# Kernel optimization log

Hardware: AMD Instinct MI355X
Metric: run time of the kernel (lower is better)

Reference implementation:

```python
import jax, jax.numpy as jnp
import numpy as np

B, S, D, H, L = 4, 4096, 64, 8, 4
VOCAB, NCLS = 256, 10
MLP = D * H          # mlp_dim = dim * heads = 512
BS = 256             # block size for banded attention
R = 256              # one-sided radius (sliding_window_size = 512)


def sinusoid_pos_emb(s, d):
    pos = np.arange(s)[:, None].astype(np.float32)
    i = np.arange(d // 2)[None, :].astype(np.float32)
    ang = pos / np.power(10000.0, 2.0 * i / d)
    pe = np.zeros((s, d), np.float32)
    pe[:, 0::2] = np.sin(ang)
    pe[:, 1::2] = np.cos(ang)
    return jnp.asarray(pe)


def layernorm(x, s, b):
    m = x.mean(-1, keepdims=True)
    v = ((x - m) ** 2).mean(-1, keepdims=True)
    return (x - m) * jax.lax.rsqrt(v + 1e-6) * s + b


def sliding_window_attn(x, wq, bq, wk, bk, wv, bv, wo, bo):
    Bx, Sx, Dx = x.shape
    Dh = Dx // H
    nb = Sx // BS

    def proj(w, b2):
        return (x @ w + b2).reshape(Bx, Sx, H, Dh).transpose(0, 2, 1, 3)

    q = proj(wq, bq) / jnp.sqrt(jnp.float32(Dh))
    k = proj(wk, bk)
    v = proj(wv, bv)

    def windows(t):  # [B,H,S,Dh] -> [B,H,nb,3*BS,Dh] (prev | self | next blocks)
        tp = jnp.pad(t, ((0, 0), (0, 0), (BS, BS), (0, 0))).reshape(Bx, H, nb + 2, BS, Dh)
        return jnp.concatenate([tp[:, :, :-2], tp[:, :, 1:-1], tp[:, :, 2:]], axis=3)

    kw, vw = windows(k), windows(v)
    qb = q.reshape(Bx, H, nb, BS, Dh)
    scores = jnp.einsum('bhnqd,bhnkd->bhnqk', qb, kw)      # [B,H,nb,BS,3*BS]

    qpos = jnp.arange(BS)[:, None]
    kpos = jnp.arange(3 * BS)[None, :] - BS
    band = jnp.abs(kpos - qpos) <= R                        # [BS,3*BS]
    kglob = jnp.arange(nb)[:, None, None] * BS + kpos[None]  # [nb,1,3*BS]
    valid = (kglob >= 0) & (kglob < Sx)
    mask = band[None] & valid                                # [nb,BS,3*BS]

    scores = jnp.where(mask[None, None], scores, jnp.float32(-1e30))
    probs = jax.nn.softmax(scores, axis=-1)
    out = jnp.einsum('bhnqk,bhnkd->bhnqd', probs, vw)
    out = out.reshape(Bx, H, Sx, Dh).transpose(0, 2, 1, 3).reshape(Bx, Sx, Dx)
    return out @ wo + bo


def setup_inputs() -> dict:
    key = jax.random.key(0)
    ks = jax.random.split(key, 12)
    g = lambda k, shp: jax.random.normal(k, shp, dtype=jnp.float32) * 0.02
    emb = g(ks[0], (VOCAB, D)).at[0].set(0.0)  # padding_idx=0 row is zeros
    return dict(
        x=jax.random.randint(ks[1], (B, S), 0, VOCAB).astype(jnp.int32),
        emb=emb,
        wq=g(ks[2], (L, D, D)), bq=jnp.zeros((L, D)),
        wk=g(ks[3], (L, D, D)), bk=jnp.zeros((L, D)),
        wv=g(ks[4], (L, D, D)), bv=jnp.zeros((L, D)),
        wo=g(ks[5], (L, D, D)), bo=jnp.zeros((L, D)),
        ln1_s=jnp.ones((L, D)), ln1_b=jnp.zeros((L, D)),
        ln2_s=jnp.ones((L, D)), ln2_b=jnp.zeros((L, D)),
        w1=g(ks[6], (L, D, MLP)), b1=jnp.zeros((L, MLP)),
        w2=g(ks[7], (L, MLP, D)), b2=jnp.zeros((L, D)),
        lnf_s=jnp.ones((D,)), lnf_b=jnp.zeros((D,)),
        wcls=g(ks[8], (D, NCLS)), bcls=jnp.zeros((NCLS,)),
    )


def reference(x, emb, wq, bq, wk, bk, wv, bv, wo, bo, ln1_s, ln1_b, ln2_s, ln2_b, w1, b1, w2, b2, lnf_s, lnf_b, wcls, bcls):
    h = emb[x] + sinusoid_pos_emb(S, D)[None]                 # embedding + fixed pos emb
    for l in range(L):
        a = sliding_window_attn(layernorm(h, ln1_s[l], ln1_b[l]),
                                wq[l], bq[l], wk[l], bk[l], wv[l], bv[l], wo[l], bo[l])
        h = h + a
        y = layernorm(h, ln2_s[l], ln2_b[l])
        y = jax.nn.gelu(y @ w1[l] + b1[l]) @ w2[l] + b2[l]
        h = h + y
    h = layernorm(h, lnf_s, lnf_b)
    pooled = h.mean(axis=1)                                   # classifier_pool='MEAN'
    return pooled @ wcls + bcls
```

## Files before the change

kernel.cpp:

```cpp
#include <hip/hip_runtime.h>
#include <hip/hip_bf16.h>

#define DEV __device__ __forceinline__

typedef __attribute__((ext_vector_type(8))) short bf16x8;
typedef __attribute__((ext_vector_type(4))) float f32x4;
typedef __attribute__((ext_vector_type(16))) float f32x16;

DEV short f2bf(float x){ __hip_bfloat16 h = __float2bfloat16(x); return *(short*)&h; }
DEV unsigned pack2bf(float a, float b){
  return (unsigned)(unsigned short)f2bf(a) | ((unsigned)(unsigned short)f2bf(b) << 16);
}
DEV float gelu_fast(float x){
  float z = 0.7978845608028654f*(x + 0.044715f*x*x*x);
  float e = __expf(-2.f*z);
  return x / (1.f + e);
}

#define SB 4096
#define NT 16384
#define DM 64

__global__ __launch_bounds__(256) void wconv(
    const float* __restrict__ wq, const float* __restrict__ wk,
    const float* __restrict__ wv, const float* __restrict__ wo,
    const float* __restrict__ w1, const float* __restrict__ w2,
    short* __restrict__ wqT, short* __restrict__ wkT,
    short* __restrict__ wvT, short* __restrict__ woT,
    short* __restrict__ w1T, short* __restrict__ w2T)
{
  int t = blockIdx.x, l = blockIdx.y;
  const float* src; short* dst; int K, N, kt, nt;
  if (t < 16) {
    int m = t >> 2, sub = t & 3; kt = sub >> 1; nt = sub & 1; K = 64; N = 64;
    const float* s4[4] = {wq, wk, wv, wo};
    short*       d4[4] = {wqT, wkT, wvT, woT};
    src = s4[m] + l*4096; dst = d4[m] + l*4096;
  } else if (t < 48) {
    kt = (t-16) >> 4; nt = (t-16) & 15; K = 64; N = 512;
    src = w1 + l*32768; dst = w1T + l*32768;
  } else {
    kt = (t-48) >> 1; nt = (t-48) & 1; K = 512; N = 64;
    src = w2 + l*32768; dst = w2T + l*32768;
  }
  __shared__ float lds[32][33];
  int tx = threadIdx.x & 31, ty = threadIdx.x >> 5;
  int k0 = kt*32, n0 = nt*32;
  #pragma unroll
  for (int j=0;j<4;++j) lds[ty+8*j][tx] = src[(size_t)(k0+ty+8*j)*N + n0 + tx];
  __syncthreads();
  #pragma unroll
  for (int j=0;j<4;++j) {
    int nn = ty+8*j;
    dst[(size_t)(n0+nn)*K + k0 + tx] = f2bf(lds[tx][nn]);
  }
}

DEV void make_frags_ln(const float* rowp, float mean, float inv,
    const float* __restrict__ s, const float* __restrict__ b, int kq,
    bf16x8& a0, bf16x8& a1){
  #pragma unroll
  for (int i=0;i<8;++i) a0[i] = f2bf((rowp[kq*8+i]-mean)*inv*s[kq*8+i]+b[kq*8+i]);
  #pragma unroll
  for (int i=0;i<8;++i) a1[i] = f2bf((rowp[32+kq*8+i]-mean)*inv*s[32+kq*8+i]+b[32+kq*8+i]);
}

template<bool EMBED, bool LAST>
__global__ __launch_bounds__(512,2) void layer_kernel(
    const int* __restrict__ x, const float* __restrict__ emb,
    const unsigned short* __restrict__ qin, const unsigned short* __restrict__ kin,
    const unsigned short* __restrict__ vin,
    const short* __restrict__ woT, const float* __restrict__ bo,
    const float* __restrict__ ln2s, const float* __restrict__ ln2b,
    const short* __restrict__ w1T, const float* __restrict__ b1,
    const short* __restrict__ w2T, const float* __restrict__ b2,
    const float* __restrict__ lns, const float* __restrict__ lnb,
    const short* __restrict__ wqT, const short* __restrict__ wkT, const short* __restrict__ wvT,
    const float* __restrict__ bq, const float* __restrict__ bk, const float* __restrict__ bv,
    unsigned short* __restrict__ qo, unsigned short* __restrict__ ko, unsigned short* __restrict__ vo,
    float* __restrict__ h, float* __restrict__ part)
{
  __shared__ uint4 regA4[4608];
  __shared__ uint4 regB4[4672];
  __shared__ float mu[64], iv[64];

  unsigned short* Ks  = (unsigned short*)regA4;
  unsigned short* abL = (unsigned short*)regA4;
  float (*hN)[68]   = (float(*)[68])((char*)regA4 + 9216);
  float (*facc)[68] = (float(*)[68])((char*)regA4 + 26624);
  unsigned short* Vs = (unsigned short*)regB4;
  short (*mid)[520]  = (short(*)[520])regB4;

  const int bid = blockIdx.x;
  const int row_g0 = bid * 64;
  const int tid = threadIdx.x;
  const int w = tid >> 6, lane = tid & 63;
  const int r = lane & 15, kq = lane >> 4;
  const int srow = tid >> 3, sd8 = tid & 7;

  if constexpr (EMBED) {
    int tg = row_g0 + srow;
    int s = tg & (SB-1);
    int tok = x[tg];
    #pragma unroll
    for (int i=0;i<8;++i) {
      int d = sd8*8 + i;
      float fe = (float)(d & ~1) * (1.0f/64.0f);
      float invk = __expf(-9.210340371976184f * fe);
      float ang = (float)s * invk;
      float pe = (d & 1) ? __cosf(ang) : __sinf(ang);
      float val = emb[tok*DM + d] + pe;
      hN[srow][d] = val;
      h[(size_t)tg*DM + d] = val;
    }
  } else {
    const int bbase = row_g0 & ~(SB-1);
    const int kwin0 = row_g0 - 256;

    for (int idx = tid; idx < 4608; idx += 512) {
      int e = idx >> 3, grp = idx & 7;
      int g = kwin0 + e;
      uint4 kv = make_uint4(0,0,0,0), vv = make_uint4(0,0,0,0);
      if ((unsigned)(g - bbase) < (unsigned)SB) {
        kv = *(const uint4*)(kin + (size_t)g*DM + grp*8);
        vv = *(const uint4*)(vin + (size_t)g*DM + grp*8);
      }
      *(uint4*)(Ks + e*64 + ((grp ^ (e & 7)) << 3)) = kv;
      const unsigned short* pv = (const unsigned short*)&vv;
      #pragma unroll
      for (int d = 0; d < 8; ++d) Vs[(grp*8 + d)*584 + e] = pv[d];
    }
    __syncthreads();

    const int qc = lane & 31;
    const int hf = lane >> 5;

    auto attn_job = [&](int qs, f32x16& oacc, float& lacc) {
      const int qglob = row_g0 + qs*32 + qc;
      bf16x8 qfrag = {};
      if (hf == 0) qfrag = *(const bf16x8*)(qin + (size_t)qglob*DM + w*8);
      for (int t = 0; t <= 16; ++t) {
        const int k0l = qs*32 + 32*t;
        const int k0g = kwin0 + k0l;
        if (k0g > bbase + SB-1 || k0g + 31 < bbase) continue;

        bf16x8 kfrag = {};
        if (hf == 0) {
          int e = k0l + qc;
          kfrag = *(const bf16x8*)(Ks + e*64 + ((w ^ (e & 7)) << 3));
        }
        f32x16 s = __builtin_amdgcn_mfma_f32_32x32x16_bf16(kfrag, qfrag, (f32x16){}, 0, 0, 0);

        float pp[16];
        bool needmask = (t == 0) | (t == 16) | (k0g < bbase) | (k0g + 31 > bbase + SB-1);
        if (needmask) {
          #pragma unroll
          for (int rr = 0; rr < 16; ++rr) {
            int klg = k0g + (rr&3) + 8*(rr>>2) + 4*hf;
            bool ok = ((unsigned)(klg - qglob + 256) <= 512u) &&
                      ((unsigned)(klg - bbase) < (unsigned)SB);
            pp[rr] = ok ? __expf(s[rr]) : 0.f;
          }
        } else {
          #pragma unroll
          for (int rr = 0; rr < 16; ++rr) pp[rr] = __expf(s[rr]);
        }
        #pragma unroll
        for (int rr = 0; rr < 16; ++rr) lacc += pp[rr];

        unsigned pk[8];
        #pragma unroll
        for (int j = 0; j < 8; ++j) pk[j] = pack2bf(pp[2*j], pp[2*j+1]);
        unsigned sw[8];
        #pragma unroll
        for (int j = 0; j < 8; ++j) sw[j] = __shfl_xor(pk[j], 32, 64);

        union { unsigned u[4]; bf16x8 v; } pbA;
        pbA.u[0] = hf ? sw[2] : pk[0];
        pbA.u[1] = hf ? sw[3] : pk[1];
        pbA.u[2] = hf ? pk[2] : sw[0];
        pbA.u[3] = hf ? pk[3] : sw[1];
        bf16x8 va1 = {};
        if (qc < 8) va1 = *(const bf16x8*)(Vs + (w*8 + qc)*584 + k0l + 8*hf);
        oacc = __builtin_amdgcn_mfma_f32_32x32x16_bf16(va1, pbA.v, oacc, 0, 0, 0);

        union { unsigned u[4]; bf16x8 v; } pbB;
        pbB.u[0] = hf ? sw[6] : pk[4];
        pbB.u[1] = hf ? sw[7] : pk[5];
        pbB.u[2] = hf ? pk[6] : sw[4];
        pbB.u[3] = hf ? pk[7] : sw[5];
        bf16x8 va2 = {};
        if (qc < 8) va2 = *(const bf16x8*)(Vs + (w*8 + qc)*584 + k0l + 16 + 8*hf);
        oacc = __builtin_amdgcn_mfma_f32_32x32x16_bf16(va2, pbB.v, oacc, 0, 0, 0);
      }
    };

    f32x16 oacc0 = {}; float la0 = 0.f;
    f32x16 oacc1 = {}; float la1 = 0.f;
    attn_job(0, oacc0, la0);
    attn_job(1, oacc1, la1);
    float rcp0 = 1.f / (la0 + __shfl_xor(la0, 32, 64));
    float rcp1 = 1.f / (la1 + __shfl_xor(la1, 32, 64));
    __syncthreads();

    {
      unsigned short ov[4];
      #pragma unroll
      for (int j = 0; j < 4; ++j) ov[j] = (unsigned short)f2bf(oacc0[j] * rcp0);
      *(uint2*)(abL + (qc)*72 + w*8 + 4*hf) = *(uint2*)ov;
      #pragma unroll
      for (int j = 0; j < 4; ++j) ov[j] = (unsigned short)f2bf(oacc1[j] * rcp1);
      *(uint2*)(abL + (32 + qc)*72 + w*8 + 4*hf) = *(uint2*)ov;
    }
    __syncthreads();

    {
      const int rh = w >> 2, ct = w & 3;
      const int col = ct*16 + r;
      const short* wp = woT + (size_t)col*64 + kq*8;
      bf16x8 wb0 = *(const bf16x8*)(wp);
      bf16x8 wb1 = *(const bf16x8*)(wp + 32);
      #pragma unroll
      for (int rf=0; rf<2; ++rf) {
        const short* abp = (const short*)(abL + (rh*32 + rf*16 + r)*72 + kq*8);
        bf16x8 a0 = *(const bf16x8*)abp;
        bf16x8 a1 = *(const bf16x8*)(abp + 32);
        f32x4 acc = (f32x4){0.f,0.f,0.f,0.f};
        acc = __builtin_amdgcn_mfma_f32_16x16x32_bf16(a0, wb0, acc, 0, 0, 0);
        acc = __builtin_amdgcn_mfma_f32_16x16x32_bf16(a1, wb1, acc, 0, 0, 0);
        #pragma unroll
        for (int j=0;j<4;++j) {
          int rl = rh*32 + rf*16 + kq*4 + j;
          hN[rl][col] = acc[j] + bo[col] + h[(size_t)(row_g0+rl)*DM + col];
        }
      }
    }
  }
  __syncthreads();

  {
    const float* p = &hN[srow][sd8*8];
    float v[8];
    float sum = 0.f;
    #pragma unroll
    for (int i=0;i<8;++i){ v[i] = p[i]; sum += v[i]; }
    sum += __shfl_xor(sum, 1, 64); sum += __shfl_xor(sum, 2, 64); sum += __shfl_xor(sum, 4, 64);
    float mean = sum * (1.f/64.f);
    float sq = 0.f;
    #pragma unroll
    for (int i=0;i<8;++i){ float d = v[i]-mean; sq += d*d; }
    sq += __shfl_xor(sq, 1, 64); sq += __shfl_xor(sq, 2, 64); sq += __shfl_xor(sq, 4, 64);
    if (sd8 == 0) { mu[srow] = mean; iv[srow] = rsqrtf(sq*(1.f/64.f) + 1e-6f); }
  }
  __syncthreads();

  if constexpr (!EMBED) {
    {
      bf16x8 a[4][2];
      #pragma unroll
      for (int rf=0; rf<4; ++rf)
        make_frags_ln(&hN[rf*16 + r][0], mu[rf*16 + r], iv[rf*16 + r], ln2s, ln2b, kq, a[rf][0], a[rf][1]);
      const int gc0 = w*64;
      bf16x8 wb[4][2];
      #pragma unroll
      for (int ct=0; ct<4; ++ct) {
        const short* wp = w1T + (size_t)(gc0 + ct*16 + r)*64 + kq*8;
        wb[ct][0] = *(const bf16x8*)(wp);
        wb[ct][1] = *(const bf16x8*)(wp + 32);
      }
      f32x4 acc1[4][4];
      #pragma unroll
      for (int ct=0;ct<4;++ct)
        #pragma unroll
        for (int rf=0;rf<4;++rf) acc1[ct][rf] = (f32x4){0.f,0.f,0.f,0.f};
      #pragma unroll
      for (int ct=0; ct<4; ++ct)
        #pragma unroll
        for (int rf=0; rf<4; ++rf) {
          acc1[ct][rf] = __builtin_amdgcn_mfma_f32_16x16x32_bf16(a[rf][0], wb[ct][0], acc1[ct][rf], 0, 0, 0);
          acc1[ct][rf] = __builtin_amdgcn_mfma_f32_16x16x32_bf16(a[rf][1], wb[ct][1], acc1[ct][rf], 0, 0, 0);
        }
      __syncthreads();
      #pragma unroll
      for (int ct=0; ct<4; ++ct) {
        int gcol = gc0 + ct*16 + r;
        float bb = b1[gcol];
        #pragma unroll
        for (int rf=0; rf<4; ++rf)
          #pragma unroll
          for (int j=0; j<4; ++j)
            mid[rf*16 + kq*4 + j][gcol] = f2bf(gelu_fast(acc1[ct][rf][j] + bb));
      }
    }
    __syncthreads();

    {
      const int kh = w >> 2, ct2 = w & 3;
      const int col2 = ct2*16 + r;
      bf16x8 wf[8];
      #pragma unroll
      for (int ks=0; ks<8; ++ks)
        wf[ks] = *(const bf16x8*)(w2T + (size_t)col2*512 + kh*256 + ks*32 + kq*8);
      f32x4 acc2[4];
      #pragma unroll
      for (int rf=0;rf<4;++rf) acc2[rf] = (f32x4){0.f,0.f,0.f,0.f};
      #pragma unroll
      for (int ks=0; ks<8; ++ks)
        #pragma unroll
        for (int rf=0; rf<4; ++rf) {
          bf16x8 af = *(const bf16x8*)(&mid[rf*16 + r][kh*256 + ks*32 + kq*8]);
          acc2[rf] = __builtin_amdgcn_mfma_f32_16x16x32_bf16(af, wf[ks], acc2[rf], 0, 0, 0);
        }
      if (kh == 0) {
        #pragma unroll
        for (int rf=0; rf<4; ++rf)
          #pragma unroll
          for (int j=0;j<4;++j)
            facc[rf*16 + kq*4 + j][col2] = acc2[rf][j];
      }
      __syncthreads();
      if (kh == 1) {
        float bb = b2[col2];
        #pragma unroll
        for (int rf=0; rf<4; ++rf)
          #pragma unroll
          for (int j=0;j<4;++j) {
            int rl = rf*16 + kq*4 + j;
            float val = acc2[rf][j] + facc[rl][col2] + bb + hN[rl][col2];
            hN[rl][col2] = val;
            h[(size_t)(row_g0+rl)*DM + col2] = val;
          }
      }
    }
    __syncthreads();

    {
      const float* p = &hN[srow][sd8*8];
      float v[8];
      float sum = 0.f;
      #pragma unroll
      for (int i=0;i<8;++i){ v[i] = p[i]; sum += v[i]; }
      sum += __shfl_xor(sum, 1, 64); sum += __shfl_xor(sum, 2, 64); sum += __shfl_xor(sum, 4, 64);
      float mean = sum * (1.f/64.f);
      float sq = 0.f;
      #pragma unroll
      for (int i=0;i<8;++i){ float d = v[i]-mean; sq += d*d; }
      sq += __shfl_xor(sq, 1, 64); sq += __shfl_xor(sq, 2, 64); sq += __shfl_xor(sq, 4, 64);
      if (sd8 == 0) { mu[srow] = mean; iv[srow] = rsqrtf(sq*(1.f/64.f) + 1e-6f); }
    }
    __syncthreads();
  }

  if constexpr (!LAST) {
    const float qscale = 0.35355339059327373f;
    bf16x8 a[4][2];
    #pragma unroll
    for (int rf=0; rf<4; ++rf)
      make_frags_ln(&hN[rf*16 + r][0], mu[rf*16 + r], iv[rf*16 + r], lns, lnb, kq, a[rf][0], a[rf][1]);
    #pragma unroll
    for (int rep=0; rep<2; ++rep) {
      int jj = w + rep*8;
      if (jj < 12) {
        int m = jj >> 2, ct = jj & 3;
        const short* WT = m==0 ? wqT : (m==1 ? wkT : wvT);
        int col = ct*16 + r;
        const short* wp = WT + (size_t)col*64 + kq*8;
        bf16x8 wb0 = *(const bf16x8*)(wp);
        bf16x8 wb1 = *(const bf16x8*)(wp + 32);
        float bias = (m==0 ? bq : (m==1 ? bk : bv))[col];
        float scale = (m==0) ? qscale : 1.f;
        unsigned short* OPT = m==0 ? qo : (m==1 ? ko : vo);
        #pragma unroll
        for (int rf=0; rf<4; ++rf) {
          f32x4 acc = (f32x4){0.f,0.f,0.f,0.f};
          acc = __builtin_amdgcn_mfma_f32_16x16x32_bf16(a[rf][0], wb0, acc, 0, 0, 0);
          acc = __builtin_amdgcn_mfma_f32_16x16x32_bf16(a[rf][1], wb1, acc, 0, 0, 0);
          #pragma unroll
          for (int j=0;j<4;++j) {
            size_t oi = (size_t)(row_g0 + rf*16 + kq*4 + j)*DM + col;
            OPT[oi] = (unsigned short)f2bf((acc[j] + bias)*scale);
          }
        }
      }
    }
  } else {
    float mean = mu[srow], inv = iv[srow];
    #pragma unroll
    for (int i=0;i<8;++i) {
      int d = sd8*8 + i;
      hN[srow][d] = (hN[srow][d]-mean)*inv*lns[d] + lnb[d];
    }
    __syncthreads();
    if (tid < 64) {
      float s = 0.f;
      #pragma unroll 4
      for (int rr=0; rr<64; ++rr) s += hN[rr][tid];
      part[bid*64 + tid] = s;
    }
  }
}

__global__ __launch_bounds__(256) void pool_finalize(const float* __restrict__ part,
    const float* __restrict__ wcls, const float* __restrict__ bcls, float* __restrict__ out)
{
  int tid = threadIdx.x;
  int b = tid >> 6, d = tid & 63;
  float sum = 0.f;
  #pragma unroll 8
  for (int i = 0; i < 64; ++i) sum += part[(b*64 + i)*64 + d];
  __shared__ float pooled[4][64];
  pooled[b][d] = sum * (1.f/4096.f);
  __syncthreads();
  if (tid < 40) {
    int bb = tid / 10, c = tid % 10;
    float acc = bcls[c];
    #pragma unroll
    for (int dd = 0; dd < 64; ++dd) acc = fmaf(pooled[bb][dd], wcls[dd*10 + c], acc);
    out[tid] = acc;
  }
}

extern "C" void kernel_launch(void* const* d_in, const int* in_sizes, int n_in,
                              void* d_out, int out_size, void* d_ws, size_t ws_size,
                              hipStream_t stream)
{
  const int*   x    = (const int*)d_in[0];
  const float* emb  = (const float*)d_in[1];
  const float* wq   = (const float*)d_in[2];
  const float* bq   = (const float*)d_in[3];
  const float* wk   = (const float*)d_in[4];
  const float* bk   = (const float*)d_in[5];
  const float* wv   = (const float*)d_in[6];
  const float* bv   = (const float*)d_in[7];
  const float* wo   = (const float*)d_in[8];
  const float* bo   = (const float*)d_in[9];
  const float* ln1s = (const float*)d_in[10];
  const float* ln1b = (const float*)d_in[11];
  const float* ln2s = (const float*)d_in[12];
  const float* ln2b = (const float*)d_in[13];
  const float* w1   = (const float*)d_in[14];
  const float* b1   = (const float*)d_in[15];
  const float* w2   = (const float*)d_in[16];
  const float* b2   = (const float*)d_in[17];
  const float* lnfs = (const float*)d_in[18];
  const float* lnfb = (const float*)d_in[19];
  const float* wcls = (const float*)d_in[20];
  const float* bcls = (const float*)d_in[21];
  float* out = (float*)d_out;

  char* wsb = (char*)d_ws;
  const size_t MB = 1u << 20;
  float* h  = (float*)(wsb);
  unsigned short* qA = (unsigned short*)(wsb + 4*MB);
  unsigned short* kA = (unsigned short*)(wsb + 6*MB);
  unsigned short* vA = (unsigned short*)(wsb + 8*MB);
  unsigned short* qB = (unsigned short*)(wsb + 10*MB);
  unsigned short* kB = (unsigned short*)(wsb + 12*MB);
  unsigned short* vB = (unsigned short*)(wsb + 14*MB);
  short* wqT = (short*)(wsb + 16*MB);
  short* wkT = (short*)(wsb + 16*MB + 32*1024);
  short* wvT = (short*)(wsb + 16*MB + 64*1024);
  short* woT = (short*)(wsb + 16*MB + 96*1024);
  short* w1T = (short*)(wsb + 16*MB + 128*1024);
  short* w2T = (short*)(wsb + 16*MB + 384*1024);
  float* part = (float*)(wsb + 17*MB);

  wconv<<<dim3(80,4),256,0,stream>>>(wq,wk,wv,wo,w1,w2, wqT,wkT,wvT,woT,w1T,w2T);

  layer_kernel<true,false><<<256,512,0,stream>>>(
      x, emb, nullptr, nullptr, nullptr,
      nullptr, nullptr, nullptr, nullptr,
      nullptr, nullptr, nullptr, nullptr,
      ln1s, ln1b,
      wqT, wkT, wvT, bq, bk, bv,
      qA, kA, vA, h, nullptr);

  for (int l = 0; l < 4; ++l) {
    unsigned short* qi = (l & 1) ? qB : qA;
    unsigned short* ki = (l & 1) ? kB : kA;
    unsigned short* vi = (l & 1) ? vB : vA;
    unsigned short* qu = (l & 1) ? qA : qB;
    unsigned short* ku = (l & 1) ? kA : kB;
    unsigned short* vu = (l & 1) ? vA : vB;
    if (l < 3) {
      layer_kernel<false,false><<<256,512,0,stream>>>(
          nullptr, nullptr, qi, ki, vi,
          woT+4096*l, bo+64*l, ln2s+64*l, ln2b+64*l,
          w1T+32768*l, b1+512*l, w2T+32768*l, b2+64*l,
          ln1s+64*(l+1), ln1b+64*(l+1),
          wqT+4096*(l+1), wkT+4096*(l+1), wvT+4096*(l+1),
          bq+64*(l+1), bk+64*(l+1), bv+64*(l+1),
          qu, ku, vu, h, nullptr);
    } else {
      layer_kernel<false,true><<<256,512,0,stream>>>(
          nullptr, nullptr, qi, ki, vi,
          woT+4096*l, bo+64*l, ln2s+64*l, ln2b+64*l,
          w1T+32768*l, b1+512*l, w2T+32768*l, b2+64*l,
          lnfs, lnfb,
          nullptr, nullptr, nullptr, nullptr, nullptr, nullptr,
          nullptr, nullptr, nullptr, h, part);
    }
  }
  pool_finalize<<<1,256,0,stream>>>(part, wcls, bcls, out);
}
```

Measured before the change: 184.3 us.

## Split embedding into lightweight kernel, fuse pool/classifier via last-block atomic, restructure V staging

The embedding plus first QKV projection moves out of the big 512-thread layer kernel into a dedicated 256-thread kernel over 32-row blocks with more blocks and lower shared-memory use. The separate pool_finalize launch is removed: the last layer block to finish, found with an atomic counter, does the mean-pool and classifier. The counter is cleared with a memset each call. V tile loading is split from K loading and reindexed so consecutive threads walk the sequence dimension, which reduces strided LDS transpose-store conflicts. The changes aim to cut launch overhead and improve occupancy of the embed stage, at the cost of an extra memset and atomic synchronisation.

```diff
diff --git a/kernel.cpp b/kernel.cpp
--- a/kernel.cpp
+++ b/kernel.cpp
@@ -65,9 +65,103 @@
   for (int i=0;i<8;++i) a1[i] = f2bf((rowp[32+kq*8+i]-mean)*inv*s[32+kq*8+i]+b[32+kq*8+i]);
 }
 
-template<bool EMBED, bool LAST>
+__global__ __launch_bounds__(256,4) void embed_head(
+    const int* __restrict__ x, const float* __restrict__ emb,
+    const float* __restrict__ lns, const float* __restrict__ lnb,
+    const short* __restrict__ wqT, const short* __restrict__ wkT, const short* __restrict__ wvT,
+    const float* __restrict__ bq, const float* __restrict__ bk, const float* __restrict__ bv,
+    unsigned short* __restrict__ qo, unsigned short* __restrict__ ko, unsigned short* __restrict__ vo,
+    float* __restrict__ h)
+{
+  __shared__ float hN[32][76];
+  __shared__ float mu[32], iv[32];
+
+  const int bid = blockIdx.x;
+  const int row_g0 = bid * 32;
+  const int tid = threadIdx.x;
+  const int w = tid >> 6, lane = tid & 63;
+  const int r = lane & 15, kq = lane >> 4;
+  const int wr0 = (w >> 1) * 16;
+  const int cc0 = (w & 1) * 32;
+  const int srow = tid >> 3, sdq = tid & 7;
+
+  bf16x8 qwb[12];
+  #pragma unroll
+  for (int m=0;m<3;++m){
+    const short* WT = m==0?wqT:(m==1?wkT:wvT);
+    const short* qp0 = WT + (size_t)(cc0 + r)*64 + kq*8;
+    const short* qp1 = WT + (size_t)(cc0 + 16 + r)*64 + kq*8;
+    qwb[4*m+0] = *(const bf16x8*)(qp0);
+    qwb[4*m+1] = *(const bf16x8*)(qp0 + 32);
+    qwb[4*m+2] = *(const bf16x8*)(qp1);
+    qwb[4*m+3] = *(const bf16x8*)(qp1 + 32);
+  }
+
+  {
+    int tg = row_g0 + srow;
+    int s = tg & (SB-1);
+    int tok = x[tg];
+    #pragma unroll
+    for (int i=0;i<8;++i) {
+      int d = sdq*8 + i;
+      float fe = (float)(d & ~1) * (1.0f/64.0f);
+      float invk = __expf(-9.210340371976184f * fe);
+      float ang = (float)s * invk;
+      float pe = (d & 1) ? __cosf(ang) : __sinf(ang);
+      float val = emb[tok*DM + d] + pe;
+      hN[srow][d] = val;
+      h[(size_t)tg*DM + d] = val;
+    }
+  }
+  __syncthreads();
+
+  {
+    const float* p = &hN[srow][sdq*8];
+    float v[8];
+    float sum = 0.f;
+    #pragma unroll
+    for (int i=0;i<8;++i){ v[i] = p[i]; sum += v[i]; }
+    sum += __shfl_xor(sum, 1, 64); sum += __shfl_xor(sum, 2, 64); sum += __shfl_xor(sum, 4, 64);
+    float mean = sum * (1.f/64.f);
+    float sq = 0.f;
+    #pragma unroll
+    for (int i=0;i<8;++i){ float d = v[i]-mean; sq += d*d; }
+    sq += __shfl_xor(sq, 1, 64); sq += __shfl_xor(sq, 2, 64); sq += __shfl_xor(sq, 4, 64);
+    if (sdq == 0) { mu[srow] = mean; iv[srow] = rsqrtf(sq*(1.f/64.f) + 1e-6f); }
+  }
+  __syncthreads();
+
+  const float qscale = 0.35355339059327373f;
+  bf16x8 a0, a1;
+  make_frags_ln(&hN[wr0+r][0], mu[wr0+r], iv[wr0+r], lns, lnb, kq, a0, a1);
+  f32x4 aq[2] = {(f32x4){0,0,0,0},(f32x4){0,0,0,0}};
+  f32x4 akk[2] = {(f32x4){0,0,0,0},(f32x4){0,0,0,0}};
+  f32x4 av[2] = {(f32x4){0,0,0,0},(f32x4){0,0,0,0}};
+  #pragma unroll
+  for (int ct=0; ct<2; ++ct) {
+    aq[ct]  = __builtin_amdgcn_mfma_f32_16x16x32_bf16(a0, qwb[0+2*ct],  aq[ct], 0, 0, 0);
+    aq[ct]  = __builtin_amdgcn_mfma_f32_16x16x32_bf16(a1, qwb[1+2*ct],  aq[ct], 0, 0, 0);
+    akk[ct] = __builtin_amdgcn_mfma_f32_16x16x32_bf16(a0, qwb[4+2*ct],  akk[ct], 0, 0, 0);
+    akk[ct] = __builtin_amdgcn_mfma_f32_16x16x32_bf16(a1, qwb[5+2*ct],  akk[ct], 0, 0, 0);
+    av[ct]  = __builtin_amdgcn_mfma_f32_16x16x32_bf16(a0, qwb[8+2*ct],  av[ct], 0, 0, 0);
+    av[ct]  = __builtin_amdgcn_mfma_f32_16x16x32_bf16(a1, qwb[9+2*ct],  av[ct], 0, 0, 0);
+  }
+  #pragma unroll
+  for (int ct=0; ct<2; ++ct) {
+    int col = cc0 + ct*16 + r;
+    float bqv = bq[col], bkv = bk[col], bvv = bv[col];
+    #pragma unroll
+    for (int j=0;j<4;++j) {
+      size_t oi = (size_t)(row_g0 + wr0 + kq*4 + j)*DM + col;
+      qo[oi] = (unsigned short)f2bf((aq[ct][j] + bqv)*qscale);
+      ko[oi] = (unsigned short)f2bf(akk[ct][j] + bkv);
+      vo[oi] = (unsigned short)f2bf(av[ct][j] + bvv);
+    }
+  }
+}
+
+template<bool LAST>
 __global__ __launch_bounds__(512,2) void layer_kernel(
-    const int* __restrict__ x, const float* __restrict__ emb,
     const unsigned short* __restrict__ qin, const unsigned short* __restrict__ kin,
     const unsigned short* __restrict__ vin,
     const short* __restrict__ woT, const float* __restrict__ bo,
@@ -78,11 +172,14 @@
     const short* __restrict__ wqT, const short* __restrict__ wkT, const short* __restrict__ wvT,
     const float* __restrict__ bq, const float* __restrict__ bk, const float* __restrict__ bv,
     unsigned short* __restrict__ qo, unsigned short* __restrict__ ko, unsigned short* __restrict__ vo,
-    float* __restrict__ h, float* __restrict__ part)
+    float* __restrict__ h, float* __restrict__ part,
+    const float* __restrict__ wcls, const float* __restrict__ bcls,
+    float* __restrict__ out, unsigned* __restrict__ cnt)
 {
   __shared__ uint4 regA4[4608];
   __shared__ uint4 regB4[4672];
   __shared__ float mu[64], iv[64];
+  __shared__ int lastflag;
 
   unsigned short* Ks  = (unsigned short*)regA4;
   unsigned short* abL = (unsigned short*)regA4;
@@ -98,40 +195,30 @@
   const int r = lane & 15, kq = lane >> 4;
   const int srow = tid >> 3, sd8 = tid & 7;
 
-  if constexpr (EMBED) {
-    int tg = row_g0 + srow;
-    int s = tg & (SB-1);
-    int tok = x[tg];
-    #pragma unroll
-    for (int i=0;i<8;++i) {
-      int d = sd8*8 + i;
-      float fe = (float)(d & ~1) * (1.0f/64.0f);
-      float invk = __expf(-9.210340371976184f * fe);
-      float ang = (float)s * invk;
-      float pe = (d & 1) ? __cosf(ang) : __sinf(ang);
-      float val = emb[tok*DM + d] + pe;
-      hN[srow][d] = val;
-      h[(size_t)tg*DM + d] = val;
-    }
-  } else {
-    const int bbase = row_g0 & ~(SB-1);
-    const int kwin0 = row_g0 - 256;
-
-    for (int idx = tid; idx < 4608; idx += 512) {
-      int e = idx >> 3, grp = idx & 7;
-      int g = kwin0 + e;
-      uint4 kv = make_uint4(0,0,0,0), vv = make_uint4(0,0,0,0);
-      if ((unsigned)(g - bbase) < (unsigned)SB) {
-        kv = *(const uint4*)(kin + (size_t)g*DM + grp*8);
-        vv = *(const uint4*)(vin + (size_t)g*DM + grp*8);
-      }
-      *(uint4*)(Ks + e*64 + ((grp ^ (e & 7)) << 3)) = kv;
-      const unsigned short* pv = (const unsigned short*)&vv;
-      #pragma unroll
-      for (int d = 0; d < 8; ++d) Vs[(grp*8 + d)*584 + e] = pv[d];
-    }
-    __syncthreads();
-
+  const int bbase = row_g0 & ~(SB-1);
+  const int kwin0 = row_g0 - 256;
+
+  for (int idx = tid; idx < 4608; idx += 512) {
+    int e = idx >> 3, grp = idx & 7;
+    int g = kwin0 + e;
+    uint4 kv = make_uint4(0,0,0,0);
+    if ((unsigned)(g - bbase) < (unsigned)SB)
+      kv = *(const uint4*)(kin + (size_t)g*DM + grp*8);
+    *(uint4*)(Ks + e*64 + ((grp ^ (e & 7)) << 3)) = kv;
+  }
+  for (int idx = tid; idx < 4608; idx += 512) {
+    int grp = idx / 576, e = idx - grp*576;
+    int g = kwin0 + e;
+    uint4 vv = make_uint4(0,0,0,0);
+    if ((unsigned)(g - bbase) < (unsigned)SB)
+      vv = *(const uint4*)(vin + (size_t)g*DM + grp*8);
+    const unsigned short* pv = (const unsigned short*)&vv;
+    #pragma unroll
+    for (int d = 0; d < 8; ++d) Vs[(grp*8 + d)*584 + e] = pv[d];
+  }
+  __syncthreads();
+
+  {
     const int qc = lane & 31;
     const int hf = lane >> 5;
 
@@ -203,36 +290,34 @@
     float rcp1 = 1.f / (la1 + __shfl_xor(la1, 32, 64));
     __syncthreads();
 
-    {
-      unsigned short ov[4];
-      #pragma unroll
-      for (int j = 0; j < 4; ++j) ov[j] = (unsigned short)f2bf(oacc0[j] * rcp0);
-      *(uint2*)(abL + (qc)*72 + w*8 + 4*hf) = *(uint2*)ov;
-      #pragma unroll
-      for (int j = 0; j < 4; ++j) ov[j] = (unsigned short)f2bf(oacc1[j] * rcp1);
-      *(uint2*)(abL + (32 + qc)*72 + w*8 + 4*hf) = *(uint2*)ov;
-    }
-    __syncthreads();
-
-    {
-      const int rh = w >> 2, ct = w & 3;
-      const int col = ct*16 + r;
-      const short* wp = woT + (size_t)col*64 + kq*8;
-      bf16x8 wb0 = *(const bf16x8*)(wp);
-      bf16x8 wb1 = *(const bf16x8*)(wp + 32);
-      #pragma unroll
-      for (int rf=0; rf<2; ++rf) {
-        const short* abp = (const short*)(abL + (rh*32 + rf*16 + r)*72 + kq*8);
-        bf16x8 a0 = *(const bf16x8*)abp;
-        bf16x8 a1 = *(const bf16x8*)(abp + 32);
-        f32x4 acc = (f32x4){0.f,0.f,0.f,0.f};
-        acc = __builtin_amdgcn_mfma_f32_16x16x32_bf16(a0, wb0, acc, 0, 0, 0);
-        acc = __builtin_amdgcn_mfma_f32_16x16x32_bf16(a1, wb1, acc, 0, 0, 0);
-        #pragma unroll
-        for (int j=0;j<4;++j) {
-          int rl = rh*32 + rf*16 + kq*4 + j;
-          hN[rl][col] = acc[j] + bo[col] + h[(size_t)(row_g0+rl)*DM + col];
-        }
+    unsigned short ov[4];
+    #pragma unroll
+    for (int j = 0; j < 4; ++j) ov[j] = (unsigned short)f2bf(oacc0[j] * rcp0);
+    *(uint2*)(abL + (qc)*72 + w*8 + 4*hf) = *(uint2*)ov;
+    #pragma unroll
+    for (int j = 0; j < 4; ++j) ov[j] = (unsigned short)f2bf(oacc1[j] * rcp1);
+    *(uint2*)(abL + (32 + qc)*72 + w*8 + 4*hf) = *(uint2*)ov;
+  }
+  __syncthreads();
+
+  {
+    const int rh = w >> 2, ct = w & 3;
+    const int col = ct*16 + r;
+    const short* wp = woT + (size_t)col*64 + kq*8;
+    bf16x8 wb0 = *(const bf16x8*)(wp);
+    bf16x8 wb1 = *(const bf16x8*)(wp + 32);
+    #pragma unroll
+    for (int rf=0; rf<2; ++rf) {
+      const short* abp = (const short*)(abL + (rh*32 + rf*16 + r)*72 + kq*8);
+      bf16x8 a0 = *(const bf16x8*)abp;
+      bf16x8 a1 = *(const bf16x8*)(abp + 32);
+      f32x4 acc = (f32x4){0.f,0.f,0.f,0.f};
+      acc = __builtin_amdgcn_mfma_f32_16x16x32_bf16(a0, wb0, acc, 0, 0, 0);
+      acc = __builtin_amdgcn_mfma_f32_16x16x32_bf16(a1, wb1, acc, 0, 0, 0);
+      #pragma unroll
+      for (int j=0;j<4;++j) {
+        int rl = rh*32 + rf*16 + kq*4 + j;
+        hN[rl][col] = acc[j] + bo[col] + h[(size_t)(row_g0+rl)*DM + col];
       }
     }
   }
@@ -254,102 +339,100 @@
   }
   __syncthreads();
 
-  if constexpr (!EMBED) {
-    {
-      bf16x8 a[4][2];
+  {
+    bf16x8 a[4][2];
+    #pragma unroll
+    for (int rf=0; rf<4; ++rf)
+      make_frags_ln(&hN[rf*16 + r][0], mu[rf*16 + r], iv[rf*16 + r], ln2s, ln2b, kq, a[rf][0], a[rf][1]);
+    const int gc0 = w*64;
+    bf16x8 wb[4][2];
+    #pragma unroll
+    for (int ct=0; ct<4; ++ct) {
+      const short* wp = w1T + (size_t)(gc0 + ct*16 + r)*64 + kq*8;
+      wb[ct][0] = *(const bf16x8*)(wp);
+      wb[ct][1] = *(const bf16x8*)(wp + 32);
+    }
+    f32x4 acc1[4][4];
+    #pragma unroll
+    for (int ct=0;ct<4;++ct)
+      #pragma unroll
+      for (int rf=0;rf<4;++rf) acc1[ct][rf] = (f32x4){0.f,0.f,0.f,0.f};
+    #pragma unroll
+    for (int ct=0; ct<4; ++ct)
+      #pragma unroll
+      for (int rf=0; rf<4; ++rf) {
+        acc1[ct][rf] = __builtin_amdgcn_mfma_f32_16x16x32_bf16(a[rf][0], wb[ct][0], acc1[ct][rf], 0, 0, 0);
+        acc1[ct][rf] = __builtin_amdgcn_mfma_f32_16x16x32_bf16(a[rf][1], wb[ct][1], acc1[ct][rf], 0, 0, 0);
+      }
+    __syncthreads();
+    #pragma unroll
+    for (int ct=0; ct<4; ++ct) {
+      int gcol = gc0 + ct*16 + r;
+      float bb = b1[gcol];
       #pragma unroll
       for (int rf=0; rf<4; ++rf)
-        make_frags_ln(&hN[rf*16 + r][0], mu[rf*16 + r], iv[rf*16 + r], ln2s, ln2b, kq, a[rf][0], a[rf][1]);
-      const int gc0 = w*64;
-      bf16x8 wb[4][2];
-      #pragma unroll
-      for (int ct=0; ct<4; ++ct) {
-        const short* wp = w1T + (size_t)(gc0 + ct*16 + r)*64 + kq*8;
-        wb[ct][0] = *(const bf16x8*)(wp);
-        wb[ct][1] = *(const bf16x8*)(wp + 32);
-      }
-      f32x4 acc1[4][4];
-      #pragma unroll
-      for (int ct=0;ct<4;++ct)
-        #pragma unroll
-        for (int rf=0;rf<4;++rf) acc1[ct][rf] = (f32x4){0.f,0.f,0.f,0.f};
-      #pragma unroll
-      for (int ct=0; ct<4; ++ct)
-        #pragma unroll
-        for (int rf=0; rf<4; ++rf) {
-          acc1[ct][rf] = __builtin_amdgcn_mfma_f32_16x16x32_bf16(a[rf][0], wb[ct][0], acc1[ct][rf], 0, 0, 0);
-          acc1[ct][rf] = __builtin_amdgcn_mfma_f32_16x16x32_bf16(a[rf][1], wb[ct][1], acc1[ct][rf], 0, 0, 0);
+        #pragma unroll
+        for (int j=0; j<4; ++j)
+          mid[rf*16 + kq*4 + j][gcol] = f2bf(gelu_fast(acc1[ct][rf][j] + bb));
+    }
+  }
+  __syncthreads();
+
+  {
+    const int kh = w >> 2, ct2 = w & 3;
+    const int col2 = ct2*16 + r;
+    bf16x8 wf[8];
+    #pragma unroll
+    for (int ks=0; ks<8; ++ks)
+      wf[ks] = *(const bf16x8*)(w2T + (size_t)col2*512 + kh*256 + ks*32 + kq*8);
+    f32x4 acc2[4];
+    #pragma unroll
+    for (int rf=0;rf<4;++rf) acc2[rf] = (f32x4){0.f,0.f,0.f,0.f};
+    #pragma unroll
+    for (int ks=0; ks<8; ++ks)
+      #pragma unroll
+      for (int rf=0; rf<4; ++rf) {
+        bf16x8 af = *(const bf16x8*)(&mid[rf*16 + r][kh*256 + ks*32 + kq*8]);
+        acc2[rf] = __builtin_amdgcn_mfma_f32_16x16x32_bf16(af, wf[ks], acc2[rf], 0, 0, 0);
+      }
+    if (kh == 0) {
+      #pragma unroll
+      for (int rf=0; rf<4; ++rf)
+        #pragma unroll
+        for (int j=0;j<4;++j)
+          facc[rf*16 + kq*4 + j][col2] = acc2[rf][j];
+    }
+    __syncthreads();
+    if (kh == 1) {
+      float bb = b2[col2];
+      #pragma unroll
+      for (int rf=0; rf<4; ++rf)
+        #pragma unroll
+        for (int j=0;j<4;++j) {
+          int rl = rf*16 + kq*4 + j;
+          float val = acc2[rf][j] + facc[rl][col2] + bb + hN[rl][col2];
+          hN[rl][col2] = val;
+          h[(size_t)(row_g0+rl)*DM + col2] = val;
         }
-      __syncthreads();
-      #pragma unroll
-      for (int ct=0; ct<4; ++ct) {
-        int gcol = gc0 + ct*16 + r;
-        float bb = b1[gcol];
-        #pragma unroll
-        for (int rf=0; rf<4; ++rf)
-          #pragma unroll
-          for (int j=0; j<4; ++j)
-            mid[rf*16 + kq*4 + j][gcol] = f2bf(gelu_fast(acc1[ct][rf][j] + bb));
-      }
-    }
-    __syncthreads();
-
-    {
-      const int kh = w >> 2, ct2 = w & 3;
-      const int col2 = ct2*16 + r;
-      bf16x8 wf[8];
-      #pragma unroll
-      for (int ks=0; ks<8; ++ks)
-        wf[ks] = *(const bf16x8*)(w2T + (size_t)col2*512 + kh*256 + ks*32 + kq*8);
-      f32x4 acc2[4];
-      #pragma unroll
-      for (int rf=0;rf<4;++rf) acc2[rf] = (f32x4){0.f,0.f,0.f,0.f};
-      #pragma unroll
-      for (int ks=0; ks<8; ++ks)
-        #pragma unroll
-        for (int rf=0; rf<4; ++rf) {
-          bf16x8 af = *(const bf16x8*)(&mid[rf*16 + r][kh*256 + ks*32 + kq*8]);
-          acc2[rf] = __builtin_amdgcn_mfma_f32_16x16x32_bf16(af, wf[ks], acc2[rf], 0, 0, 0);
-        }
-      if (kh == 0) {
-        #pragma unroll
-        for (int rf=0; rf<4; ++rf)
-          #pragma unroll
-          for (int j=0;j<4;++j)
-            facc[rf*16 + kq*4 + j][col2] = acc2[rf][j];
-      }
-      __syncthreads();
-      if (kh == 1) {
-        float bb = b2[col2];
-        #pragma unroll
-        for (int rf=0; rf<4; ++rf)
-          #pragma unroll
-          for (int j=0;j<4;++j) {
-            int rl = rf*16 + kq*4 + j;
-            float val = acc2[rf][j] + facc[rl][col2] + bb + hN[rl][col2];
-            hN[rl][col2] = val;
-            h[(size_t)(row_g0+rl)*DM + col2] = val;
-          }
-      }
-    }
-    __syncthreads();
-
-    {
-      const float* p = &hN[srow][sd8*8];
-      float v[8];
-      float sum = 0.f;
-      #pragma unroll
-      for (int i=0;i<8;++i){ v[i] = p[i]; sum += v[i]; }
-      sum += __shfl_xor(sum, 1, 64); sum += __shfl_xor(sum, 2, 64); sum += __shfl_xor(sum, 4, 64);
-      float mean = sum * (1.f/64.f);
-      float sq = 0.f;
-      #pragma unroll
-      for (int i=0;i<8;++i){ float d = v[i]-mean; sq += d*d; }
-      sq += __shfl_xor(sq, 1, 64); sq += __shfl_xor(sq, 2, 64); sq += __shfl_xor(sq, 4, 64);
-      if (sd8 == 0) { mu[srow] = mean; iv[srow] = rsqrtf(sq*(1.f/64.f) + 1e-6f); }
-    }
-    __syncthreads();
-  }
+    }
+  }
+  __syncthreads();
+
+  {
+    const float* p = &hN[srow][sd8*8];
+    float v[8];
+    float sum = 0.f;
+    #pragma unroll
+    for (int i=0;i<8;++i){ v[i] = p[i]; sum += v[i]; }
+    sum += __shfl_xor(sum, 1, 64); sum += __shfl_xor(sum, 2, 64); sum += __shfl_xor(sum, 4, 64);
+    float mean = sum * (1.f/64.f);
+    float sq = 0.f;
+    #pragma unroll
+    for (int i=0;i<8;++i){ float d = v[i]-mean; sq += d*d; }
+    sq += __shfl_xor(sq, 1, 64); sq += __shfl_xor(sq, 2, 64); sq += __shfl_xor(sq, 4, 64);
+    if (sd8 == 0) { mu[srow] = mean; iv[srow] = rsqrtf(sq*(1.f/64.f) + 1e-6f); }
+  }
+  __syncthreads();
 
   if constexpr (!LAST) {
     const float qscale = 0.35355339059327373f;
@@ -397,26 +480,33 @@
       for (int rr=0; rr<64; ++rr) s += hN[rr][tid];
       part[bid*64 + tid] = s;
     }
-  }
-}
-
-__global__ __launch_bounds__(256) void pool_finalize(const float* __restrict__ part,
-    const float* __restrict__ wcls, const float* __restrict__ bcls, float* __restrict__ out)
-{
-  int tid = threadIdx.x;
-  int b = tid >> 6, d = tid & 63;
-  float sum = 0.f;
-  #pragma unroll 8
-  for (int i = 0; i < 64; ++i) sum += part[(b*64 + i)*64 + d];
-  __shared__ float pooled[4][64];
-  pooled[b][d] = sum * (1.f/4096.f);
-  __syncthreads();
-  if (tid < 40) {
-    int bb = tid / 10, c = tid % 10;
-    float acc = bcls[c];
-    #pragma unroll
-    for (int dd = 0; dd < 64; ++dd) acc = fmaf(pooled[bb][dd], wcls[dd*10 + c], acc);
-    out[tid] = acc;
+    __syncthreads();
+
+    if (tid == 0) {
+      __threadfence();
+      unsigned old = atomicAdd(cnt, 1u);
+      lastflag = (old == 255u) ? 1 : 0;
+    }
+    __syncthreads();
+    if (lastflag) {
+      __threadfence();
+      float* pool = &hN[0][0];
+      if (tid < 256) {
+        int b = tid >> 6, d = tid & 63;
+        float sum = 0.f;
+        #pragma unroll 8
+        for (int i = 0; i < 64; ++i) sum += part[(b*64 + i)*64 + d];
+        pool[b*64 + d] = sum * (1.f/4096.f);
+      }
+      __syncthreads();
+      if (tid < 40) {
+        int bb = tid / 10, c = tid % 10;
+        float acc = bcls[c];
+        #pragma unroll
+        for (int dd = 0; dd < 64; ++dd) acc = fmaf(pool[bb*64 + dd], wcls[dd*10 + c], acc);
+        out[tid] = acc;
+      }
+    }
   }
 }
 
@@ -464,16 +554,13 @@
   short* w1T = (short*)(wsb + 16*MB + 128*1024);
   short* w2T = (short*)(wsb + 16*MB + 384*1024);
   float* part = (float*)(wsb + 17*MB);
-
+  unsigned* cnt = (unsigned*)(wsb + 17*MB + 64*1024);
+
+  hipMemsetAsync((void*)cnt, 0, 64, stream);
   wconv<<<dim3(80,4),256,0,stream>>>(wq,wk,wv,wo,w1,w2, wqT,wkT,wvT,woT,w1T,w2T);
 
-  layer_kernel<true,false><<<256,512,0,stream>>>(
-      x, emb, nullptr, nullptr, nullptr,
-      nullptr, nullptr, nullptr, nullptr,
-      nullptr, nullptr, nullptr, nullptr,
-      ln1s, ln1b,
-      wqT, wkT, wvT, bq, bk, bv,
-      qA, kA, vA, h, nullptr);
+  embed_head<<<512,256,0,stream>>>(
+      x, emb, ln1s, ln1b, wqT, wkT, wvT, bq, bk, bv, qA, kA, vA, h);
 
   for (int l = 0; l < 4; ++l) {
     unsigned short* qi = (l & 1) ? qB : qA;
@@ -483,23 +570,22 @@
     unsigned short* ku = (l & 1) ? kA : kB;
     unsigned short* vu = (l & 1) ? vA : vB;
     if (l < 3) {
-      layer_kernel<false,false><<<256,512,0,stream>>>(
-          nullptr, nullptr, qi, ki, vi,
+      layer_kernel<false><<<256,512,0,stream>>>(
+          qi, ki, vi,
           woT+4096*l, bo+64*l, ln2s+64*l, ln2b+64*l,
           w1T+32768*l, b1+512*l, w2T+32768*l, b2+64*l,
           ln1s+64*(l+1), ln1b+64*(l+1),
           wqT+4096*(l+1), wkT+4096*(l+1), wvT+4096*(l+1),
           bq+64*(l+1), bk+64*(l+1), bv+64*(l+1),
-          qu, ku, vu, h, nullptr);
+          qu, ku, vu, h, nullptr, nullptr, nullptr, nullptr, nullptr);
     } else {
-      layer_kernel<false,true><<<256,512,0,stream>>>(
-          nullptr, nullptr, qi, ki, vi,
+      layer_kernel<true><<<256,512,0,stream>>>(
+          qi, ki, vi,
           woT+4096*l, bo+64*l, ln2s+64*l, ln2b+64*l,
           w1T+32768*l, b1+512*l, w2T+32768*l, b2+64*l,
           lnfs, lnfb,
           nullptr, nullptr, nullptr, nullptr, nullptr, nullptr,
-          nullptr, nullptr, nullptr, h, part);
-    }
-  }
-  pool_finalize<<<1,256,0,stream>>>(part, wcls, bcls, out);
-}
+          nullptr, nullptr, nullptr, h, part, wcls, bcls, out, cnt);
+    }
+  }
+}
```

Result: slower. 206.9 us (+12.2%).
